# Optimization experiments

Measured on AMD Instinct MI355X. Metric: run time of the kernel, lower is better.

## Reference

```python
import jax, jax.numpy as jnp
import numpy as np
import math

B, S, D, H = 4, 2048, 1024, 16
DK = D // H

def setup_inputs() -> dict:
    key = jax.random.key(0)
    ks = jax.random.split(key, 12)
    scale = 1.0 / math.sqrt(D)
    inp = {
        "query": jax.random.normal(ks[0], (B, S, D), jnp.float32),
        "key_": jax.random.normal(ks[1], (B, S, D), jnp.float32),
        "value": jax.random.normal(ks[2], (B, S, D), jnp.float32),
        "mask": jnp.broadcast_to(jnp.tril(jnp.ones((S, S), jnp.int32)), (B, S, S)),
        "Wq": jax.random.normal(ks[3], (D, D), jnp.float32) * scale,
        "bq": jnp.zeros((D,), jnp.float32),
        "Wk": jax.random.normal(ks[4], (D, D), jnp.float32) * scale,
        "bk": jnp.zeros((D,), jnp.float32),
        "Wv": jax.random.normal(ks[5], (D, D), jnp.float32) * scale,
        "bv": jnp.zeros((D,), jnp.float32),
        "Wo": jax.random.normal(ks[6], (D, D), jnp.float32) * scale,
        "bo": jnp.zeros((D,), jnp.float32),
    }
    return inp

def reference(query, key_, value, mask, Wq, bq, Wk, bk, Wv, bv, Wo, bo):
    # Linear projections (torch Linear: x @ W^T + b), split into heads [B,H,S,DK]
    def proj(x, W, b):
        y = jnp.einsum('bsd,ed->bse', x, W) + b
        return y.reshape(B, S, H, DK).transpose(0, 2, 1, 3)
    Q = proj(query, Wq, bq)
    K = proj(key_, Wk, bk)
    V = proj(value, Wv, bv)
    # scaled dot-product attention with additive mask-fill
    scores = jnp.einsum('bhqd,bhkd->bhqk', Q, K) / math.sqrt(DK)
    scores = jnp.where(mask[:, None, :, :] == 0, jnp.float32(-1e9), scores)
    attn = jax.nn.softmax(scores, axis=-1)  # dropout p=0.0 (eval) -> identity
    ctx = jnp.einsum('bhqk,bhkd->bhqd', attn, V)
    ctx = ctx.transpose(0, 2, 1, 3).reshape(B, S, D)
    out = jnp.einsum('bsd,ed->bse', ctx, Wo) + bo
    return out
```

## Files before the change

### kernel.cpp

```cpp
#include <hip/hip_runtime.h>
#include <hip/hip_bf16.h>
#include <cstdint>
#include <cstddef>

static constexpr int kB = 4, kS = 2048, kD = 1024, kH = 16, kDK = 64;
static constexpr int kM = kB * kS;

typedef __attribute__((ext_vector_type(8))) __bf16 bf16x8;
typedef __attribute__((ext_vector_type(4))) float f32x4;

#define MFMA_BF16(a, b, c) __builtin_amdgcn_mfma_f32_16x16x32_bf16((a), (b), (c), 0, 0, 0)

#define GLDS16(gp, lp)                                                        \
  __builtin_amdgcn_global_load_lds(                                           \
      (__attribute__((address_space(1))) void*)(gp),                          \
      (__attribute__((address_space(3))) void*)(lp), 16, 0, 0)

__device__ __forceinline__ bf16x8 cvt8(const float* s, int i) {
  const float4 a = ((const float4*)s)[i * 2 + 0];
  const float4 b = ((const float4*)s)[i * 2 + 1];
  bf16x8 o;
  o[0] = (__bf16)a.x; o[1] = (__bf16)a.y; o[2] = (__bf16)a.z; o[3] = (__bf16)a.w;
  o[4] = (__bf16)b.x; o[5] = (__bf16)b.y; o[6] = (__bf16)b.z; o[7] = (__bf16)b.w;
  return o;
}

__global__ __launch_bounds__(256) void cvt_f32_bf16(
    const float* __restrict__ src, __bf16* __restrict__ dst, int n8) {
  const int i = blockIdx.x * 256 + threadIdx.x;
  if (i >= n8) return;
  ((bf16x8*)dst)[i] = cvt8(src, i);
}

__global__ __launch_bounds__(256) void cvt_act3(
    const float* __restrict__ a, const float* __restrict__ b,
    const float* __restrict__ c, __bf16* __restrict__ da,
    __bf16* __restrict__ db, __bf16* __restrict__ dc) {
  const int seg = blockIdx.x >> 12;
  const int i = (blockIdx.x & 4095) * 256 + threadIdx.x;
  const float* s = seg == 0 ? a : seg == 1 ? b : c;
  __bf16* d = seg == 0 ? da : seg == 1 ? db : dc;
  ((bf16x8*)d)[i] = cvt8(s, i);
}

__global__ __launch_bounds__(256) void cvt_w4(
    const float* __restrict__ a, const float* __restrict__ b,
    const float* __restrict__ c, const float* __restrict__ d,
    __bf16* __restrict__ da, __bf16* __restrict__ db,
    __bf16* __restrict__ dc, __bf16* __restrict__ dd) {
  const int seg = blockIdx.x >> 9;
  const int i = (blockIdx.x & 511) * 256 + threadIdx.x;
  const float* s = seg == 0 ? a : seg == 1 ? b : seg == 2 ? c : d;
  __bf16* o = seg == 0 ? da : seg == 1 ? db : seg == 2 ? dc : dd;
  ((bf16x8*)o)[i] = cvt8(s, i);
}

template <typename OutT>
__device__ __forceinline__ void gemm_core(
    const __bf16* __restrict__ A, const __bf16* __restrict__ W,
    const float* __restrict__ bias, OutT* __restrict__ out, int mode, int bid,
    __bf16* As, __bf16* Ws) {
  const int tid = threadIdx.x;
  const int wave = tid >> 6, lane = tid & 63;
  const int col = lane & 15, quad = lane >> 4;
  const int m0 = (bid & 63) * 128;
  const int n0 = (bid >> 6) * 128;
  const int wr = (wave & 1) * 64, wc = (wave >> 1) * 64;

  f32x4 acc[4][4] = {};

  int srow[4], sgo[4];
#pragma unroll
  for (int i = 0; i < 4; ++i) {
    const int s = i * 256 + tid;
    srow[i] = s >> 3;
    sgo[i] = (((s & 7) ^ ((s >> 3) & 7))) * 8;
  }
  const int g0 = ((quad) ^ (col & 7)) * 16;
  const int g1 = ((quad + 4) ^ (col & 7)) * 16;

  for (int k0 = 0; k0 < 1024; k0 += 64) {
#pragma unroll
    for (int i = 0; i < 4; ++i) {
      GLDS16(A + (size_t)(m0 + srow[i]) * 1024 + k0 + sgo[i],
             (char*)As + i * 4096 + wave * 1024);
      GLDS16(W + (size_t)(n0 + srow[i]) * 1024 + k0 + sgo[i],
             (char*)Ws + i * 4096 + wave * 1024);
    }
    __syncthreads();
#pragma unroll
    for (int h = 0; h < 2; ++h) {
      const int go = h ? g1 : g0;
      bf16x8 af[4], wf[4];
#pragma unroll
      for (int t = 0; t < 4; ++t) {
        af[t] = *(const bf16x8*)((const char*)As + (wr + t * 16 + col) * 128 + go);
        wf[t] = *(const bf16x8*)((const char*)Ws + (wc + t * 16 + col) * 128 + go);
      }
#pragma unroll
      for (int rt = 0; rt < 4; ++rt)
#pragma unroll
        for (int ct = 0; ct < 4; ++ct)
          acc[rt][ct] = MFMA_BF16(af[rt], wf[ct], acc[rt][ct]);
    }
    __syncthreads();
  }

#pragma unroll
  for (int ct = 0; ct < 4; ++ct) {
    const int n = n0 + wc + ct * 16 + col;
    const float bb = bias[n];
#pragma unroll
    for (int rt = 0; rt < 4; ++rt) {
#pragma unroll
      for (int r = 0; r < 4; ++r) {
        const int m = m0 + wr + rt * 16 + quad * 4 + r;
        const float v = acc[rt][ct][r] + bb;
        size_t idx;
        if (mode == 0) {
          idx = (size_t)m * 1024 + n;
        } else {
          const int b = m >> 11, s = m & 2047;
          const int h = n >> 6, dk = n & 63;
          if (mode == 1)
            idx = ((size_t)(b * 16 + h) * 2048 + s) * 64 + dk;
          else
            idx = ((size_t)(b * 16 + h) * 64 + dk) * 2048 + s;
        }
        out[idx] = (OutT)v;
      }
    }
  }
}

template <int MODE, typename OutT>
__global__ __launch_bounds__(256) void gemm_one(
    const __bf16* __restrict__ A, const __bf16* __restrict__ W,
    const float* __restrict__ bias, OutT* __restrict__ out) {
  __shared__ __align__(16) __bf16 As[128 * 64];
  __shared__ __align__(16) __bf16 Ws[128 * 64];
  gemm_core<OutT>(A, W, bias, out, MODE, blockIdx.x, As, Ws);
}

#define READQ(B_, QM_, QN_)                                                   \
  do {                                                                        \
    const char* Ab_ = (const char*)As8 + ((B_) * 2 + (QM_)) * 16384 + rowA;   \
    const char* Bb_ = (const char*)Bs8 + ((B_) * 2 + (QN_)) * 16384 + rowB;   \
    _Pragma("unroll") for (int mi = 0; mi < 4; ++mi) {                        \
      af[mi][0] = *(const bf16x8*)(Ab_ + mi * 2048 + gb0);                    \
      af[mi][1] = *(const bf16x8*)(Ab_ + mi * 2048 + gb1);                    \
    }                                                                         \
    _Pragma("unroll") for (int ni = 0; ni < 2; ++ni) {                        \
      bfrag[ni][0] = *(const bf16x8*)(Bb_ + ni * 2048 + gb0);                 \
      bfrag[ni][1] = *(const bf16x8*)(Bb_ + ni * 2048 + gb1);                 \
    }                                                                         \
  } while (0)

#define MFMAQ(QM_, QN_)                                                       \
  do {                                                                        \
    __builtin_amdgcn_s_barrier();                                             \
    asm volatile("s_waitcnt lgkmcnt(0)" ::: "memory");                        \
    __builtin_amdgcn_s_setprio(1);                                            \
    _Pragma("unroll") for (int mi = 0; mi < 4; ++mi) {                        \
      _Pragma("unroll") for (int ni = 0; ni < 2; ++ni) {                      \
        f32x4& a_ = acc[(QM_) * 4 + mi][(QN_) * 2 + ni];                      \
        a_ = MFMA_BF16(af[mi][0], bfrag[ni][0], a_);                          \
        a_ = MFMA_BF16(af[mi][1], bfrag[ni][1], a_);                          \
      }                                                                       \
    }                                                                         \
    __builtin_amdgcn_s_setprio(0);                                            \
    __builtin_amdgcn_s_barrier();                                             \
  } while (0)

#define STAGE_A8(B_, H_, KT_)                                                 \
  do {                                                                        \
    char* d_ = (char*)As8 + ((B_) * 2 + (H_)) * 16384 + wave * 1024;          \
    GLDS16(A + (size_t)(m0 + (H_) * 128 + srow) * 1024 + (KT_) * 64 + sgo,    \
           d_);                                                               \
    GLDS16(A + (size_t)(m0 + (H_) * 128 + 64 + srow) * 1024 + (KT_) * 64 +    \
               sgo,                                                           \
           d_ + 8192);                                                        \
  } while (0)

#define STAGE_B8(B_, H_, KT_)                                                 \
  do {                                                                        \
    char* d_ = (char*)Bs8 + ((B_) * 2 + (H_)) * 16384 + wave * 1024;          \
    GLDS16(W + (size_t)(n0 + (H_) * 128 + srow) * 1024 + (KT_) * 64 + sgo,    \
           d_);                                                               \
    GLDS16(W + (size_t)(n0 + (H_) * 128 + 64 + srow) * 1024 + (KT_) * 64 +    \
               sgo,                                                           \
           d_ + 8192);                                                        \
  } while (0)

__global__ __launch_bounds__(512, 2) void gemm_qkv8(
    const __bf16* __restrict__ Aq, const __bf16* __restrict__ Ak,
    const __bf16* __restrict__ Av, const __bf16* __restrict__ Wqb,
    const __bf16* __restrict__ Wkb, const __bf16* __restrict__ Wvb,
    const float* __restrict__ bq, const float* __restrict__ bk,
    const float* __restrict__ bv, __bf16* __restrict__ Qw,
    __bf16* __restrict__ Kw, __bf16* __restrict__ Vw) {
  __shared__ __align__(16) __bf16 As8[2][2][128 * 64];
  __shared__ __align__(16) __bf16 Bs8[2][2][128 * 64];

  int bid = (blockIdx.x & 7) * 48 + (blockIdx.x >> 3);
  const int seg = bid >> 7;
  bid &= 127;
  const int m0 = (bid & 31) * 256;
  const int n0 = (bid >> 5) * 256;

  const __bf16* __restrict__ A = seg == 0 ? Aq : seg == 1 ? Ak : Av;
  const __bf16* __restrict__ W = seg == 0 ? Wqb : seg == 1 ? Wkb : Wvb;
  const float* __restrict__ bias = seg == 0 ? bq : seg == 1 ? bk : bv;
  __bf16* __restrict__ out = seg == 0 ? Qw : seg == 1 ? Kw : Vw;
  const int mode = (seg == 2) ? 2 : 1;

  const int tid = threadIdx.x;
  const int wave = tid >> 6, lane = tid & 63;
  const int col = lane & 15, quad = lane >> 4;
  const int wm = wave >> 2, wn = wave & 3;

  const int srow = tid >> 3;
  const int sgo = ((tid & 7) ^ (srow & 7)) * 8;
  const int gb0 = ((quad) ^ (col & 7)) * 16;
  const int gb1 = ((quad + 4) ^ (col & 7)) * 16;
  const int rowA = (wm * 64 + col) * 128;
  const int rowB = (wn * 32 + col) * 128;

  f32x4 acc[8][4] = {};
  bf16x8 af[4][2], bfrag[2][2];

  STAGE_A8(0, 0, 0);
  STAGE_B8(0, 0, 0);
  STAGE_A8(0, 1, 0);
  STAGE_B8(0, 1, 0);
  STAGE_A8(1, 0, 1);
  STAGE_B8(1, 0, 1);
  asm volatile("s_waitcnt vmcnt(4)" ::: "memory");
  __builtin_amdgcn_s_barrier();

#pragma unroll 2
  for (int t = 0; t < 16; ++t) {
    const int buf = t & 1;
    READQ(buf, 0, 0);
    if (t < 15)
      STAGE_A8(buf ^ 1, 1, t + 1);
    else
      asm volatile("s_waitcnt vmcnt(0)" ::: "memory");
    MFMAQ(0, 0);
    READQ(buf, 0, 1);
    if (t < 15) STAGE_B8(buf ^ 1, 1, t + 1);
    MFMAQ(0, 1);
    READQ(buf, 1, 0);
    if (t < 14) STAGE_A8(buf, 0, t + 2);
    MFMAQ(1, 0);
    READQ(buf, 1, 1);
    if (t < 14) STAGE_B8(buf, 0, t + 2);
    asm volatile("s_waitcnt vmcnt(4)" ::: "memory");
    MFMAQ(1, 1);
  }

#pragma unroll
  for (int an = 0; an < 4; ++an) {
    const int n = n0 + (an >> 1) * 128 + wn * 32 + (an & 1) * 16 + col;
    const float bb = bias[n];
    const int hh = n >> 6, dk = n & 63;
#pragma unroll
    for (int am = 0; am < 8; ++am) {
#pragma unroll
      for (int r = 0; r < 4; ++r) {
        const int m =
            m0 + (am >> 2) * 128 + wm * 64 + (am & 3) * 16 + quad * 4 + r;
        const int b_ = m >> 11, s_ = m & 2047;
        const size_t idx =
            (mode == 1) ? ((size_t)(b_ * 16 + hh) * 2048 + s_) * 64 + dk
                        : ((size_t)(b_ * 16 + hh) * 64 + dk) * 2048 + s_;
        out[idx] = (__bf16)(acc[am][an][r] + bb);
      }
    }
  }
}

#undef READQ
#undef MFMAQ
#undef STAGE_A8
#undef STAGE_B8

__global__ __launch_bounds__(256, 4) void flash_attn(
    const __bf16* __restrict__ Q, const __bf16* __restrict__ K,
    const __bf16* __restrict__ Vt, __bf16* __restrict__ ctx) {
  __shared__ __align__(16) __bf16 Ks[64 * 64];
  __shared__ __align__(16) __bf16 Vs[64 * 64];
  __shared__ __align__(16) __bf16 Pb[4][2][16 * 72];

  const int tid = threadIdx.x;
  const int wave = tid >> 6, lane = tid & 63;
  const int col = lane & 15, quad = lane >> 4;
  const int bh = blockIdx.x >> 4;
  const int pair = blockIdx.x & 15;
  const int b = bh >> 4, h = bh & 15;
  const int t_lo = pair, t_hi = 31 - pair;
  const int q0f[2] = {t_lo * 64 + wave * 16, t_hi * 64 + wave * 16};

  constexpr float SCL = 0.18033688011112042f;

  bf16x8 qf[2][2];
#pragma unroll
  for (int f = 0; f < 2; ++f) {
    const __bf16* Qp = Q + ((size_t)bh * kS + q0f[f] + col) * 64 + quad * 8;
    qf[f][0] = *(const bf16x8*)Qp;
    qf[f][1] = *(const bf16x8*)(Qp + 32);
  }

  f32x4 o[2][4] = {};
  f32x4 lacc[2] = {};
  bf16x8 ones;
#pragma unroll
  for (int i = 0; i < 8; ++i) ones[i] = (__bf16)1.0f;

  const __bf16* Kg = K + (size_t)bh * kS * 64;
  const __bf16* Vg = Vt + (size_t)bh * 64 * kS;

  const int row0 = tid >> 3, g0 = (tid & 7) ^ (row0 & 7);
  const int row1 = (256 + tid) >> 3, g1 = (tid & 7) ^ (row1 & 7);
  char* KsB = (char*)Ks + wave * 1024;
  char* VsB = (char*)Vs + wave * 1024;

  const int fgoff0 = ((quad) ^ (col & 7)) * 16;
  const int fgoff1 = ((quad + 4) ^ (col & 7)) * 16;
  const int maskbase = wave * 16 + quad * 4;

  __bf16* Pw0 = &Pb[wave][0][0];
  __bf16* Pw1 = &Pb[wave][1][0];
  const __bf16* Pr0 = Pw0 + col * 72 + quad * 8;
  const __bf16* Pr1 = Pw1 + col * 72 + quad * 8;

  auto body = [&](int c, bool lo, bool d0, bool d1) {
    const int k0 = c * 64;
    GLDS16(Kg + (size_t)(k0 + row0) * 64 + g0 * 8, KsB);
    GLDS16(Vg + (size_t)row0 * kS + k0 + g0 * 8, VsB);
    GLDS16(Kg + (size_t)(k0 + row1) * 64 + g1 * 8, KsB + 4096);
    GLDS16(Vg + (size_t)row1 * kS + k0 + g1 * 8, VsB + 4096);
    __syncthreads();

    f32x4 s[2][4];
#pragma unroll
    for (int kt = 0; kt < 4; ++kt) {
      const char* kp = (const char*)Ks + (kt * 16 + col) * 128;
      const bf16x8 kf0 = *(const bf16x8*)(kp + fgoff0);
      const bf16x8 kf1 = *(const bf16x8*)(kp + fgoff1);
      f32x4 z = {};
      s[1][kt] = MFMA_BF16(qf[1][1], kf1, MFMA_BF16(qf[1][0], kf0, z));
      if (lo) s[0][kt] = MFMA_BF16(qf[0][1], kf1, MFMA_BF16(qf[0][0], kf0, z));
    }
#pragma unroll
    for (int kt = 0; kt < 4; ++kt) {
#pragma unroll
      for (int r = 0; r < 4; ++r) {
        float pv1 = __builtin_amdgcn_exp2f(s[1][kt][r] * SCL);
        if (d1 && (kt * 16 + col > maskbase + r)) pv1 = 0.0f;
        Pw1[(quad * 4 + r) * 72 + kt * 16 + col] = (__bf16)pv1;
        if (lo) {
          float pv0 = __builtin_amdgcn_exp2f(s[0][kt][r] * SCL);
          if (d0 && (kt * 16 + col > maskbase + r)) pv0 = 0.0f;
          Pw0[(quad * 4 + r) * 72 + kt * 16 + col] = (__bf16)pv0;
        }
      }
    }
    __threadfence_block();
    const bf16x8 pf1a = *(const bf16x8*)Pr1;
    const bf16x8 pf1b = *(const bf16x8*)(Pr1 + 32);
    bf16x8 pf0a = {}, pf0b = {};
    if (lo) {
      pf0a = *(const bf16x8*)Pr0;
      pf0b = *(const bf16x8*)(Pr0 + 32);
    }
#pragma unroll
    for (int dt = 0; dt < 4; ++dt) {
      const char* vp = (const char*)Vs + (dt * 16 + col) * 128;
      const bf16x8 vf0 = *(const bf16x8*)(vp + fgoff0);
      const bf16x8 vf1 = *(const bf16x8*)(vp + fgoff1);
      o[1][dt] = MFMA_BF16(pf1b, vf1, MFMA_BF16(pf1a, vf0, o[1][dt]));
      if (lo) o[0][dt] = MFMA_BF16(pf0b, vf1, MFMA_BF16(pf0a, vf0, o[0][dt]));
    }
    lacc[1] = MFMA_BF16(pf1b, ones, MFMA_BF16(pf1a, ones, lacc[1]));
    if (lo) lacc[0] = MFMA_BF16(pf0b, ones, MFMA_BF16(pf0a, ones, lacc[0]));
    __syncthreads();
  };

  for (int c = 0; c <= t_lo; ++c) body(c, true, c == t_lo, false);
  for (int c = t_lo + 1; c <= t_hi; ++c) body(c, false, false, c == t_hi);

#pragma unroll
  for (int f = 0; f < 2; ++f) {
#pragma unroll
    for (int r = 0; r < 4; ++r) {
      const float inv = 1.0f / lacc[f][r];
      const int srow = q0f[f] + quad * 4 + r;
      __bf16* cp = ctx + ((size_t)b * kS + srow) * kD + h * 64 + col;
#pragma unroll
      for (int dt = 0; dt < 4; ++dt)
        cp[dt * 16] = (__bf16)(o[f][dt][r] * inv);
    }
  }
}

extern "C" void kernel_launch(void* const* d_in, const int* in_sizes, int n_in,
                              void* d_out, int out_size, void* d_ws, size_t ws_size,
                              hipStream_t stream) {
  const float* query = (const float*)d_in[0];
  const float* key_  = (const float*)d_in[1];
  const float* value = (const float*)d_in[2];
  const float* Wq = (const float*)d_in[4];
  const float* bq = (const float*)d_in[5];
  const float* Wk = (const float*)d_in[6];
  const float* bk = (const float*)d_in[7];
  const float* Wv = (const float*)d_in[8];
  const float* bv = (const float*)d_in[9];
  const float* Wo = (const float*)d_in[10];
  const float* bo = (const float*)d_in[11];

  const size_t e = (size_t)kM * kD;
  const size_t w = (size_t)kD * kD;
  float* out = (float*)d_out;

  const size_t REQ = (6 * e + 4 * w) * sizeof(__bf16);

  if (ws_size >= REQ) {
    __bf16* Qw  = (__bf16*)d_ws;
    __bf16* Kw  = Qw + e;
    __bf16* Vw  = Kw + e;
    __bf16* Aq  = Vw + e;
    __bf16* Ak  = Aq + e;
    __bf16* Av  = Ak + e;
    __bf16* Wqb = Av + e;
    __bf16* Wkb = Wqb + w;
    __bf16* Wvb = Wkb + w;
    __bf16* Wob = Wvb + w;

    cvt_act3<<<3 * 4096, 256, 0, stream>>>(query, key_, value, Aq, Ak, Av);
    cvt_w4<<<4 * 512, 256, 0, stream>>>(Wq, Wk, Wv, Wo, Wqb, Wkb, Wvb, Wob);
    gemm_qkv8<<<384, 512, 0, stream>>>(Aq, Ak, Av, Wqb, Wkb, Wvb, bq, bk, bv,
                                       Qw, Kw, Vw);
    flash_attn<<<kB * kH * 16, 256, 0, stream>>>(Qw, Kw, Vw, Aq);
    gemm_one<0, float><<<512, 256, 0, stream>>>(Aq, Wob, bo, out);
  } else {
    __bf16* Qw = (__bf16*)d_ws;
    __bf16* Kw = Qw + e;
    __bf16* Vw = Kw + e;
    __bf16* Ab = Vw + e;
    __bf16* Wb = Ab + e;

    const int actg = (int)(e / 8 / 256);
    const int wg = (int)(w / 8 / 256);
    cvt_f32_bf16<<<actg, 256, 0, stream>>>(query, Ab, (int)(e / 8));
    cvt_f32_bf16<<<wg, 256, 0, stream>>>(Wq, Wb, (int)(w / 8));
    gemm_one<1, __bf16><<<512, 256, 0, stream>>>(Ab, Wb, bq, Qw);
    cvt_f32_bf16<<<actg, 256, 0, stream>>>(key_, Ab, (int)(e / 8));
    cvt_f32_bf16<<<wg, 256, 0, stream>>>(Wk, Wb, (int)(w / 8));
    gemm_one<1, __bf16><<<512, 256, 0, stream>>>(Ab, Wb, bk, Kw);
    cvt_f32_bf16<<<actg, 256, 0, stream>>>(value, Ab, (int)(e / 8));
    cvt_f32_bf16<<<wg, 256, 0, stream>>>(Wv, Wb, (int)(w / 8));
    gemm_one<2, __bf16><<<512, 256, 0, stream>>>(Ab, Wb, bv, Vw);
    flash_attn<<<kB * kH * 16, 256, 0, stream>>>(Qw, Kw, Vw, Ab);
    cvt_f32_bf16<<<wg, 256, 0, stream>>>(Wo, Wb, (int)(w / 8));
    gemm_one<0, float><<<512, 256, 0, stream>>>(Ab, Wb, bo, out);
  }
}
```

Baseline: 403.6 us.

## Rewrite QKV GEMM main loop with explicit buffers and split A/B fragment reads

Replaces the rolled, runtime-buffer-indexed K loop of the fused QKV projection GEMM with a manually unrolled two-stage schedule that uses compile-time buffer indices. A fragments are no longer re-read from LDS when only the B quadrant changes, which cuts LDS traffic. A sched_barrier pins the MFMA block so the compiler cannot reorder it. The global-load wait is folded into the quadrant's trailing barrier, and an explicit tail is added. The blockIdx swizzle that spread segments across XCDs is dropped, which may change L2 locality.

```diff
diff --git a/kernel.cpp b/kernel.cpp
--- a/kernel.cpp
+++ b/kernel.cpp
@@ -142,37 +142,25 @@
   gemm_core<OutT>(A, W, bias, out, MODE, blockIdx.x, As, Ws);
 }
 
-#define READQ(B_, QM_, QN_)                                                   \
+#define READA(B_, QM_)                                                        \
   do {                                                                        \
     const char* Ab_ = (const char*)As8 + ((B_) * 2 + (QM_)) * 16384 + rowA;   \
-    const char* Bb_ = (const char*)Bs8 + ((B_) * 2 + (QN_)) * 16384 + rowB;   \
     _Pragma("unroll") for (int mi = 0; mi < 4; ++mi) {                        \
       af[mi][0] = *(const bf16x8*)(Ab_ + mi * 2048 + gb0);                    \
       af[mi][1] = *(const bf16x8*)(Ab_ + mi * 2048 + gb1);                    \
     }                                                                         \
+  } while (0)
+
+#define READB(B_, QN_)                                                        \
+  do {                                                                        \
+    const char* Bb_ = (const char*)Bs8 + ((B_) * 2 + (QN_)) * 16384 + rowB;   \
     _Pragma("unroll") for (int ni = 0; ni < 2; ++ni) {                        \
       bfrag[ni][0] = *(const bf16x8*)(Bb_ + ni * 2048 + gb0);                 \
       bfrag[ni][1] = *(const bf16x8*)(Bb_ + ni * 2048 + gb1);                 \
     }                                                                         \
   } while (0)
 
-#define MFMAQ(QM_, QN_)                                                       \
-  do {                                                                        \
-    __builtin_amdgcn_s_barrier();                                             \
-    asm volatile("s_waitcnt lgkmcnt(0)" ::: "memory");                        \
-    __builtin_amdgcn_s_setprio(1);                                            \
-    _Pragma("unroll") for (int mi = 0; mi < 4; ++mi) {                        \
-      _Pragma("unroll") for (int ni = 0; ni < 2; ++ni) {                      \
-        f32x4& a_ = acc[(QM_) * 4 + mi][(QN_) * 2 + ni];                      \
-        a_ = MFMA_BF16(af[mi][0], bfrag[ni][0], a_);                          \
-        a_ = MFMA_BF16(af[mi][1], bfrag[ni][1], a_);                          \
-      }                                                                       \
-    }                                                                         \
-    __builtin_amdgcn_s_setprio(0);                                            \
-    __builtin_amdgcn_s_barrier();                                             \
-  } while (0)
-
-#define STAGE_A8(B_, H_, KT_)                                                 \
+#define STAGE_AH(B_, H_, KT_)                                                 \
   do {                                                                        \
     char* d_ = (char*)As8 + ((B_) * 2 + (H_)) * 16384 + wave * 1024;          \
     GLDS16(A + (size_t)(m0 + (H_) * 128 + srow) * 1024 + (KT_) * 64 + sgo,    \
@@ -182,7 +170,7 @@
            d_ + 8192);                                                        \
   } while (0)
 
-#define STAGE_B8(B_, H_, KT_)                                                 \
+#define STAGE_BH(B_, H_, KT_)                                                 \
   do {                                                                        \
     char* d_ = (char*)Bs8 + ((B_) * 2 + (H_)) * 16384 + wave * 1024;          \
     GLDS16(W + (size_t)(n0 + (H_) * 128 + srow) * 1024 + (KT_) * 64 + sgo,    \
@@ -190,6 +178,35 @@
     GLDS16(W + (size_t)(n0 + (H_) * 128 + 64 + srow) * 1024 + (KT_) * 64 +    \
                sgo,                                                           \
            d_ + 8192);                                                        \
+  } while (0)
+
+#define MFMAQ_BODY(QM_, QN_)                                                  \
+  __builtin_amdgcn_s_barrier();                                               \
+  asm volatile("s_waitcnt lgkmcnt(0)" ::: "memory");                          \
+  __builtin_amdgcn_sched_barrier(0);                                          \
+  __builtin_amdgcn_s_setprio(1);                                              \
+  _Pragma("unroll") for (int mi = 0; mi < 4; ++mi) {                          \
+    _Pragma("unroll") for (int ni = 0; ni < 2; ++ni) {                        \
+      f32x4& a_ = acc[(QM_) * 4 + mi][(QN_) * 2 + ni];                        \
+      a_ = MFMA_BF16(af[mi][0], bfrag[ni][0], a_);                            \
+      a_ = MFMA_BF16(af[mi][1], bfrag[ni][1], a_);                            \
+    }                                                                         \
+  }                                                                           \
+  __builtin_amdgcn_s_setprio(0);
+
+#define MFMAQ(QM_, QN_)                                                       \
+  do {                                                                        \
+    MFMAQ_BODY(QM_, QN_)                                                      \
+    __builtin_amdgcn_s_barrier();                                             \
+    asm volatile("" ::: "memory");                                            \
+  } while (0)
+
+#define MFMAQ_W(QM_, QN_, N_)                                                 \
+  do {                                                                        \
+    MFMAQ_BODY(QM_, QN_)                                                      \
+    asm volatile("s_waitcnt vmcnt(" #N_ ")" ::: "memory");                    \
+    __builtin_amdgcn_s_barrier();                                             \
+    asm volatile("" ::: "memory");                                            \
   } while (0)
 
 __global__ __launch_bounds__(512, 2) void gemm_qkv8(
@@ -202,9 +219,8 @@
   __shared__ __align__(16) __bf16 As8[2][2][128 * 64];
   __shared__ __align__(16) __bf16 Bs8[2][2][128 * 64];
 
-  int bid = (blockIdx.x & 7) * 48 + (blockIdx.x >> 3);
-  const int seg = bid >> 7;
-  bid &= 127;
+  const int seg = blockIdx.x >> 7;
+  const int bid = blockIdx.x & 127;
   const int m0 = (bid & 31) * 256;
   const int n0 = (bid >> 5) * 256;
 
@@ -229,35 +245,35 @@
   f32x4 acc[8][4] = {};
   bf16x8 af[4][2], bfrag[2][2];
 
-  STAGE_A8(0, 0, 0);
-  STAGE_B8(0, 0, 0);
-  STAGE_A8(0, 1, 0);
-  STAGE_B8(0, 1, 0);
-  STAGE_A8(1, 0, 1);
-  STAGE_B8(1, 0, 1);
+  STAGE_AH(0, 0, 0);
+  STAGE_BH(0, 0, 0);
+  STAGE_AH(0, 1, 0);
+  STAGE_BH(0, 1, 0);
+  STAGE_AH(1, 0, 1);
+  STAGE_BH(1, 0, 1);
   asm volatile("s_waitcnt vmcnt(4)" ::: "memory");
   __builtin_amdgcn_s_barrier();
-
-#pragma unroll 2
-  for (int t = 0; t < 16; ++t) {
-    const int buf = t & 1;
-    READQ(buf, 0, 0);
-    if (t < 15)
-      STAGE_A8(buf ^ 1, 1, t + 1);
-    else
-      asm volatile("s_waitcnt vmcnt(0)" ::: "memory");
-    MFMAQ(0, 0);
-    READQ(buf, 0, 1);
-    if (t < 15) STAGE_B8(buf ^ 1, 1, t + 1);
-    MFMAQ(0, 1);
-    READQ(buf, 1, 0);
-    if (t < 14) STAGE_A8(buf, 0, t + 2);
-    MFMAQ(1, 0);
-    READQ(buf, 1, 1);
-    if (t < 14) STAGE_B8(buf, 0, t + 2);
-    asm volatile("s_waitcnt vmcnt(4)" ::: "memory");
-    MFMAQ(1, 1);
-  }
+  asm volatile("" ::: "memory");
+
+  for (int i = 0; i < 7; ++i) {
+    const int kt1 = 2 * i + 1, kt2 = 2 * i + 2, kt3 = 2 * i + 3;
+    READA(0, 0); READB(0, 0); STAGE_AH(1, 1, kt1); MFMAQ(0, 0);
+    READB(0, 1);              STAGE_BH(1, 1, kt1); MFMAQ(0, 1);
+    READA(0, 1); READB(0, 0); STAGE_AH(0, 0, kt2); MFMAQ(1, 0);
+    READB(0, 1);              STAGE_BH(0, 0, kt2); MFMAQ_W(1, 1, 4);
+    READA(1, 0); READB(1, 0); STAGE_AH(0, 1, kt2); MFMAQ(0, 0);
+    READB(1, 1);              STAGE_BH(0, 1, kt2); MFMAQ(0, 1);
+    READA(1, 1); READB(1, 0); STAGE_AH(1, 0, kt3); MFMAQ(1, 0);
+    READB(1, 1);              STAGE_BH(1, 0, kt3); MFMAQ_W(1, 1, 4);
+  }
+  READA(0, 0); READB(0, 0); STAGE_AH(1, 1, 15); MFMAQ(0, 0);
+  READB(0, 1);              STAGE_BH(1, 1, 15); MFMAQ(0, 1);
+  READA(0, 1); READB(0, 0);                     MFMAQ(1, 0);
+  READB(0, 1);                                  MFMAQ_W(1, 1, 0);
+  READA(1, 0); READB(1, 0);                     MFMAQ(0, 0);
+  READB(1, 1);                                  MFMAQ(0, 1);
+  READA(1, 1); READB(1, 0);                     MFMAQ(1, 0);
+  READB(1, 1);                                  MFMAQ(1, 1);
 
 #pragma unroll
   for (int an = 0; an < 4; ++an) {
@@ -280,10 +296,13 @@
   }
 }
 
-#undef READQ
+#undef READA
+#undef READB
+#undef STAGE_AH
+#undef STAGE_BH
+#undef MFMAQ_BODY
 #undef MFMAQ
-#undef STAGE_A8
-#undef STAGE_B8
+#undef MFMAQ_W
 
 __global__ __launch_bounds__(256, 4) void flash_attn(
     const __bf16* __restrict__ Q, const __bf16* __restrict__ K,
```

Measured after the change: 373.1 us. -7.6%, faster.
